# Kernel optimization log

Measured on AMD Instinct MI355X. Metric: run time of the kernel, lower is better.

The kernel has to match this reference:

```python
import jax, jax.numpy as jnp
import numpy as np

# World configuration (2D layout ['h','w'])
B = 16            # batch
NH, NW = 64, 64   # token grid (token_sizes)
DO = 768          # dim_in + dim_coords
KH, KW = 16, 16   # kernel_sizes (patch extent, overlapping)
SH, SW = 8, 8     # patch_sizes (strides)
H, WF = 512, 512  # field_sizes
E = H * WF        # world.num_elements


def _build_fold_index():
    # idx[h, w, dh, dw] = clamp(h*SH+dh, 0, H-1)*WF + clamp(w*SW+dw, 0, WF-1)
    # mirrors FieldDecoder._build_fold_index with grid strides (WF, 1)
    ph = np.clip(np.arange(NH)[:, None] * SH + np.arange(KH)[None, :], 0, H - 1)   # [NH,KH]
    pw = np.clip(np.arange(NW)[:, None] * SW + np.arange(KW)[None, :], 0, WF - 1)  # [NW,KW]
    idx = ph[:, None, :, None] * WF + pw[None, :, None, :]                          # [NH,NW,KH,KW]
    return jnp.asarray(idx.reshape(-1), dtype=jnp.int32)


def setup_inputs() -> dict:
    key = jax.random.key(0)
    k1, k2 = jax.random.split(key)
    tgt = jax.random.normal(k1, (B, NH * NW, DO), dtype=jnp.float32)
    weight = jax.random.normal(k2, (KH, KW, DO), dtype=jnp.float32) * 0.02  # EinMix weight (k=v=1 absorbed)
    idx = _build_fold_index()
    return {"tgt": tgt, "weight": weight, "idx": idx}


def reference(tgt, weight, idx):
    # EinMix: 'b (h w) do -> b (h w hh ww)'  (shared per-patch projection, k=v=1)
    proj = jnp.einsum('bnd,xyd->bnxy', tgt, weight)          # [B, NH*NW, KH, KW]
    proj = proj.reshape(B, -1)                                # flat order (h, w, hh, ww) == idx layout
    # scatter_reduce(reduce='mean', include_self=False): sum then divide by counts
    sums = jnp.zeros((B, E), proj.dtype).at[:, idx].add(proj)
    counts = jnp.zeros((E,), proj.dtype).at[idx].add(1.0)     # every element is covered (kernel >= stride)
    field = sums / jnp.maximum(counts, 1.0)
    # unflatten_fields: 'b (flat) -> b h w'
    return field.reshape(B, H, WF)
```

## Files before the change

kernel.cpp:

```cpp
#include <hip/hip_runtime.h>
#include <hip/hip_bf16.h>

#define DIM      768
#define NPATCH   4096
#define BATCH    16
#define MROWS    65536
#define NCOLS    256

typedef __attribute__((ext_vector_type(8))) short bf16x8;
typedef __attribute__((ext_vector_type(4))) float f32x4;
typedef unsigned short ushort_t;

static __device__ __forceinline__ unsigned short f2bf(float f) {
    union { float f; unsigned int u; } v; v.f = f;
    unsigned int u = v.u;
    return (unsigned short)((u + 0x7FFFu + ((u >> 16) & 1u)) >> 16);
}
static __device__ __forceinline__ float bf2f(unsigned int u16) {
    union { unsigned int i; float f; } x; x.i = u16 << 16; return x.f;
}

__global__ void wconv_kernel(const float* __restrict__ w, unsigned short* __restrict__ wb) {
    int i = blockIdx.x * blockDim.x + threadIdx.x;
    float4 v = ((const float4*)w)[i];
    unsigned int p0 = (unsigned)f2bf(v.x) | ((unsigned)f2bf(v.y) << 16);
    unsigned int p1 = (unsigned)f2bf(v.z) | ((unsigned)f2bf(v.w) << 16);
    ((uint2*)wb)[i] = make_uint2(p0, p1);
}

#define KHALF 384
#define LSTRA 392
#define CSTR  264

__global__ __launch_bounds__(256, 3) void gemm_kernel(const float* __restrict__ A,
                                                      const unsigned short* __restrict__ Bw,
                                                      unsigned short* __restrict__ Cb) {
    __shared__ unsigned short sA[64 * LSTRA];

    const int tid  = threadIdx.x;
    const int m0   = blockIdx.x * 64;
    const int wave = tid >> 6;
    const int lane = tid & 63;
    const int l15  = lane & 15;
    const int quad = lane >> 4;
    const int n0w  = wave * 64;

    f32x4 acc[4][4] = {};

    const int srow = tid >> 2;
    const int su   = tid & 3;

    const unsigned short* bBase[4];
    #pragma unroll
    for (int j = 0; j < 4; ++j)
        bBase[j] = Bw + (size_t)(n0w + j * 16 + l15) * DIM + quad * 8;
    const unsigned short* aBase = sA + l15 * LSTRA + quad * 8;

    for (int half = 0; half < 2; ++half) {
        const int kbase = half * KHALF;
        __syncthreads();
        {
            const float* aRow = A + (size_t)(m0 + srow) * DIM + kbase + su * 4;
            unsigned short* dRow = sA + srow * LSTRA + su * 4;
            #pragma unroll
            for (int p = 0; p < 24; ++p) {
                float4 v = *(const float4*)(aRow + p * 16);
                unsigned int p0 = (unsigned)f2bf(v.x) | ((unsigned)f2bf(v.y) << 16);
                unsigned int p1 = (unsigned)f2bf(v.z) | ((unsigned)f2bf(v.w) << 16);
                *(uint2*)(dRow + p * 16) = make_uint2(p0, p1);
            }
        }
        __syncthreads();

        #pragma unroll 4
        for (int kk = 0; kk < 12; ++kk) {
            bf16x8 bfr[4];
            #pragma unroll
            for (int j = 0; j < 4; ++j)
                bfr[j] = *(const bf16x8*)(bBase[j] + kbase + kk * 32);
            bf16x8 af[4];
            #pragma unroll
            for (int i = 0; i < 4; ++i)
                af[i] = *(const bf16x8*)(aBase + i * 16 * LSTRA + kk * 32);
            #pragma unroll
            for (int i = 0; i < 4; ++i)
                #pragma unroll
                for (int j = 0; j < 4; ++j)
                    acc[i][j] = __builtin_amdgcn_mfma_f32_16x16x32_bf16(af[i], bfr[j], acc[i][j], 0, 0, 0);
        }
    }

    __syncthreads();
    unsigned short* sC = sA;
    #pragma unroll
    for (int i = 0; i < 4; ++i)
        #pragma unroll
        for (int j = 0; j < 4; ++j)
            #pragma unroll
            for (int rr = 0; rr < 4; ++rr)
                sC[(i * 16 + quad * 4 + rr) * CSTR + n0w + j * 16 + l15] = f2bf(acc[i][j][rr]);
    __syncthreads();

    const int orow = tid >> 2;
    const int ou   = tid & 3;
    #pragma unroll
    for (int p = 0; p < 8; ++p) {
        uint4 v = *(const uint4*)(&sC[orow * CSTR + ou * 64 + p * 8]);
        *(uint4*)(Cb + (size_t)(m0 + orow) * NCOLS + ou * 64 + p * 8) = v;
    }
}

__global__ __launch_bounds__(256) void gather_kernel(const unsigned short* __restrict__ proj,
                                                     float* __restrict__ out) {
    __shared__ unsigned short sPrev[64 * 256];
    __shared__ unsigned short sCur[64 * 256];

    const int blk = blockIdx.x;
    const int b   = blk >> 6;
    const int h   = blk & 63;
    const int tid = threadIdx.x;
    const unsigned short* base = proj + (size_t)b * (NPATCH * NCOLS);

    const uint4* gCur = (const uint4*)(base + (size_t)h * 64 * 256);
    #pragma unroll
    for (int p = 0; p < 8; ++p)
        ((uint4*)sCur)[tid + p * 256] = gCur[tid + p * 256];
    if (h > 0) {
        const uint4* gPrev = (const uint4*)(base + (size_t)(h - 1) * 64 * 256);
        #pragma unroll
        for (int p = 0; p < 8; ++p)
            ((uint4*)sPrev)[tid + p * 256] = gPrev[tid + p * 256];
    }
    __syncthreads();

    const int r  = tid >> 5;
    const int cg = tid & 31;
    const int ph = h * 8 + r;

    auto tapW = [&](const unsigned short* row, int dh, int pw) -> float {
        const int w1 = pw >> 3, dw = pw & 7;
        float v = bf2f(row[w1 * 256 + dh * 16 + dw]);
        if (pw >= 8)
            v += bf2f(row[(w1 - 1) * 256 + dh * 16 + dw + 8]);
        if (pw == 511) {
            #pragma unroll
            for (int dwe = 8; dwe < 16; ++dwe)
                v += bf2f(row[63 * 256 + dh * 16 + dwe]);
        }
        return v;
    };

    const float inv_ch = (h == 0) ? 1.f : ((ph == 511) ? 0.1f : 0.5f);

    float res[16];
    #pragma unroll
    for (int j = 0; j < 16; ++j) {
        const int pw = cg * 16 + j;
        float v = tapW(sCur, r, pw);
        if (h > 0) v += tapW(sPrev, r + 8, pw);
        if (ph == 511) {
            #pragma unroll
            for (int dh = 8; dh < 16; ++dh) v += tapW(sCur, dh, pw);
        }
        const float inv_cw = (pw < 8) ? 1.f : ((pw == 511) ? 0.1f : 0.5f);
        res[j] = v * inv_ch * inv_cw;
    }

    float* orow = out + ((size_t)(b * 512 + ph)) * 512 + cg * 16;
    #pragma unroll
    for (int q = 0; q < 4; ++q)
        *(float4*)(orow + q * 4) = make_float4(res[4 * q], res[4 * q + 1], res[4 * q + 2], res[4 * q + 3]);
}

extern "C" void kernel_launch(void* const* d_in, const int* in_sizes, int n_in,
                              void* d_out, int out_size, void* d_ws, size_t ws_size,
                              hipStream_t stream) {
    const float* tgt    = (const float*)d_in[0];
    const float* weight = (const float*)d_in[1];
    float* out = (float*)d_out;

    unsigned short* proj = (unsigned short*)d_ws;
    unsigned short* wbf  = (unsigned short*)((char*)d_ws + (size_t)MROWS * NCOLS * 2);

    wconv_kernel<<<192, 256, 0, stream>>>(weight, wbf);
    gemm_kernel<<<MROWS / 64, 256, 0, stream>>>(tgt, wbf, proj);
    gather_kernel<<<BATCH * 64, 256, 0, stream>>>(proj, out);
}
```

Measured before the change: 371.9 us.

## Shrink GEMM tile to 32 rows with K-chunking; load only needed prev-row half in gather

The GEMM now uses a 32-row M tile and streams the K dimension in six 128-wide chunks through a small LDS buffer, which cuts registers and LDS so more blocks fit per CU (launch bound raised to 6). The trade is twice as many blocks and more reloads of the weight fragments, plus a barrier per chunk with no overlap of loads and compute. The gather kernel now loads only the lower-half kernel rows (dh 8..15) of the previous patch row, halving that global read and its LDS footprint.

```diff
diff --git a/kernel.cpp b/kernel.cpp
--- a/kernel.cpp
+++ b/kernel.cpp
@@ -9,7 +9,6 @@
 
 typedef __attribute__((ext_vector_type(8))) short bf16x8;
 typedef __attribute__((ext_vector_type(4))) float f32x4;
-typedef unsigned short ushort_t;
 
 static __device__ __forceinline__ unsigned short f2bf(float f) {
     union { float f; unsigned int u; } v; v.f = f;
@@ -28,92 +27,85 @@
     ((uint2*)wb)[i] = make_uint2(p0, p1);
 }
 
-#define KHALF 384
-#define LSTRA 392
-#define CSTR  264
+#define CHUNK 128
+#define LSTC  136
 
-__global__ __launch_bounds__(256, 3) void gemm_kernel(const float* __restrict__ A,
+__global__ __launch_bounds__(256, 6) void gemm_kernel(const float* __restrict__ A,
                                                       const unsigned short* __restrict__ Bw,
                                                       unsigned short* __restrict__ Cb) {
-    __shared__ unsigned short sA[64 * LSTRA];
+    __shared__ unsigned short smem[32 * 256];
 
     const int tid  = threadIdx.x;
-    const int m0   = blockIdx.x * 64;
-    const int wave = tid >> 6;
+    const int m0   = blockIdx.x * 32;
+    const int wv   = tid >> 6;
     const int lane = tid & 63;
     const int l15  = lane & 15;
     const int quad = lane >> 4;
-    const int n0w  = wave * 64;
 
-    f32x4 acc[4][4] = {};
-
-    const int srow = tid >> 2;
-    const int su   = tid & 3;
+    f32x4 acc[2][4] = {};
 
     const unsigned short* bBase[4];
     #pragma unroll
     for (int j = 0; j < 4; ++j)
-        bBase[j] = Bw + (size_t)(n0w + j * 16 + l15) * DIM + quad * 8;
-    const unsigned short* aBase = sA + l15 * LSTRA + quad * 8;
+        bBase[j] = Bw + (size_t)(wv * 64 + j * 16 + l15) * DIM + quad * 8;
+    const unsigned short* aFrag0 = smem + l15 * LSTC + quad * 8;
+    const unsigned short* aFrag1 = aFrag0 + 16 * LSTC;
 
-    for (int half = 0; half < 2; ++half) {
-        const int kbase = half * KHALF;
+    const int srow = tid >> 3;
+    const int su   = tid & 7;
+    const float* aSrc = A + (size_t)(m0 + srow) * DIM + su * 4;
+    unsigned short* aDst = smem + srow * LSTC + su * 4;
+
+    for (int c = 0; c < 6; ++c) {
+        const int kb = c * CHUNK;
         __syncthreads();
-        {
-            const float* aRow = A + (size_t)(m0 + srow) * DIM + kbase + su * 4;
-            unsigned short* dRow = sA + srow * LSTRA + su * 4;
-            #pragma unroll
-            for (int p = 0; p < 24; ++p) {
-                float4 v = *(const float4*)(aRow + p * 16);
-                unsigned int p0 = (unsigned)f2bf(v.x) | ((unsigned)f2bf(v.y) << 16);
-                unsigned int p1 = (unsigned)f2bf(v.z) | ((unsigned)f2bf(v.w) << 16);
-                *(uint2*)(dRow + p * 16) = make_uint2(p0, p1);
-            }
+        #pragma unroll
+        for (int p = 0; p < 4; ++p) {
+            float4 v = *(const float4*)(aSrc + kb + p * 32);
+            unsigned int p0 = (unsigned)f2bf(v.x) | ((unsigned)f2bf(v.y) << 16);
+            unsigned int p1 = (unsigned)f2bf(v.z) | ((unsigned)f2bf(v.w) << 16);
+            *(uint2*)(aDst + p * 32) = make_uint2(p0, p1);
         }
         __syncthreads();
-
-        #pragma unroll 4
-        for (int kk = 0; kk < 12; ++kk) {
-            bf16x8 bfr[4];
+        #pragma unroll
+        for (int kk = 0; kk < 4; ++kk) {
+            bf16x8 bf[4];
             #pragma unroll
             for (int j = 0; j < 4; ++j)
-                bfr[j] = *(const bf16x8*)(bBase[j] + kbase + kk * 32);
-            bf16x8 af[4];
+                bf[j] = *(const bf16x8*)(bBase[j] + kb + kk * 32);
+            bf16x8 a0 = *(const bf16x8*)(aFrag0 + kk * 32);
+            bf16x8 a1 = *(const bf16x8*)(aFrag1 + kk * 32);
             #pragma unroll
-            for (int i = 0; i < 4; ++i)
-                af[i] = *(const bf16x8*)(aBase + i * 16 * LSTRA + kk * 32);
-            #pragma unroll
-            for (int i = 0; i < 4; ++i)
-                #pragma unroll
-                for (int j = 0; j < 4; ++j)
-                    acc[i][j] = __builtin_amdgcn_mfma_f32_16x16x32_bf16(af[i], bfr[j], acc[i][j], 0, 0, 0);
+            for (int j = 0; j < 4; ++j) {
+                acc[0][j] = __builtin_amdgcn_mfma_f32_16x16x32_bf16(a0, bf[j], acc[0][j], 0, 0, 0);
+                acc[1][j] = __builtin_amdgcn_mfma_f32_16x16x32_bf16(a1, bf[j], acc[1][j], 0, 0, 0);
+            }
         }
     }
 
     __syncthreads();
-    unsigned short* sC = sA;
     #pragma unroll
-    for (int i = 0; i < 4; ++i)
+    for (int i = 0; i < 2; ++i)
         #pragma unroll
         for (int j = 0; j < 4; ++j)
             #pragma unroll
             for (int rr = 0; rr < 4; ++rr)
-                sC[(i * 16 + quad * 4 + rr) * CSTR + n0w + j * 16 + l15] = f2bf(acc[i][j][rr]);
+                smem[(i * 16 + quad * 4 + rr) * 256 + wv * 64 + j * 16 + l15] = f2bf(acc[i][j][rr]);
     __syncthreads();
 
-    const int orow = tid >> 2;
-    const int ou   = tid & 3;
+    const int orow = tid >> 3;
+    const int ou   = tid & 7;
     #pragma unroll
-    for (int p = 0; p < 8; ++p) {
-        uint4 v = *(const uint4*)(&sC[orow * CSTR + ou * 64 + p * 8]);
-        *(uint4*)(Cb + (size_t)(m0 + orow) * NCOLS + ou * 64 + p * 8) = v;
+    for (int q = 0; q < 4; ++q) {
+        uint4 v = *(const uint4*)(smem + orow * 256 + ou * 32 + q * 8);
+        *(uint4*)(Cb + (size_t)(m0 + orow) * NCOLS + ou * 32 + q * 8) = v;
     }
 }
 
 __global__ __launch_bounds__(256) void gather_kernel(const unsigned short* __restrict__ proj,
                                                      float* __restrict__ out) {
-    __shared__ unsigned short sPrev[64 * 256];
     __shared__ unsigned short sCur[64 * 256];
+    __shared__ unsigned short sPrevHi[64 * 128];
 
     const int blk = blockIdx.x;
     const int b   = blk >> 6;
@@ -128,39 +120,48 @@
     if (h > 0) {
         const uint4* gPrev = (const uint4*)(base + (size_t)(h - 1) * 64 * 256);
         #pragma unroll
-        for (int p = 0; p < 8; ++p)
-            ((uint4*)sPrev)[tid + p * 256] = gPrev[tid + p * 256];
+        for (int p = 0; p < 4; ++p) {
+            int i = tid + p * 256;
+            ((uint4*)sPrevHi)[i] = gPrev[(i >> 4) * 32 + 16 + (i & 15)];
+        }
     }
     __syncthreads();
 
     const int r  = tid >> 5;
     const int cg = tid & 31;
     const int ph = h * 8 + r;
-
-    auto tapW = [&](const unsigned short* row, int dh, int pw) -> float {
-        const int w1 = pw >> 3, dw = pw & 7;
-        float v = bf2f(row[w1 * 256 + dh * 16 + dw]);
-        if (pw >= 8)
-            v += bf2f(row[(w1 - 1) * 256 + dh * 16 + dw + 8]);
-        if (pw == 511) {
-            #pragma unroll
-            for (int dwe = 8; dwe < 16; ++dwe)
-                v += bf2f(row[63 * 256 + dh * 16 + dwe]);
-        }
-        return v;
-    };
-
     const float inv_ch = (h == 0) ? 1.f : ((ph == 511) ? 0.1f : 0.5f);
 
     float res[16];
     #pragma unroll
     for (int j = 0; j < 16; ++j) {
         const int pw = cg * 16 + j;
-        float v = tapW(sCur, r, pw);
-        if (h > 0) v += tapW(sPrev, r + 8, pw);
+        const int w1 = pw >> 3, dw = pw & 7;
+        float v = bf2f(sCur[w1 * 256 + r * 16 + dw]);
+        if (pw >= 8) v += bf2f(sCur[(w1 - 1) * 256 + r * 16 + dw + 8]);
+        if (h > 0) {
+            v += bf2f(sPrevHi[w1 * 128 + r * 16 + dw]);
+            if (pw >= 8) v += bf2f(sPrevHi[(w1 - 1) * 128 + r * 16 + dw + 8]);
+        }
+        if (pw == 511) {
+            #pragma unroll
+            for (int dwe = 8; dwe < 16; ++dwe) {
+                v += bf2f(sCur[63 * 256 + r * 16 + dwe]);
+                if (h > 0) v += bf2f(sPrevHi[63 * 128 + r * 16 + dwe]);
+            }
+        }
         if (ph == 511) {
-            #pragma unroll
-            for (int dh = 8; dh < 16; ++dh) v += tapW(sCur, dh, pw);
+            #pragma unroll 1
+            for (int dh = 8; dh < 16; ++dh) {
+                float e = bf2f(sCur[w1 * 256 + dh * 16 + dw]);
+                if (pw >= 8) e += bf2f(sCur[(w1 - 1) * 256 + dh * 16 + dw + 8]);
+                if (pw == 511) {
+                    #pragma unroll
+                    for (int dwe = 8; dwe < 16; ++dwe)
+                        e += bf2f(sCur[63 * 256 + dh * 16 + dwe]);
+                }
+                v += e;
+            }
         }
         const float inv_cw = (pw < 8) ? 1.f : ((pw == 511) ? 0.1f : 0.5f);
         res[j] = v * inv_ch * inv_cw;
@@ -183,6 +184,6 @@
     unsigned short* wbf  = (unsigned short*)((char*)d_ws + (size_t)MROWS * NCOLS * 2);
 
     wconv_kernel<<<192, 256, 0, stream>>>(weight, wbf);
-    gemm_kernel<<<MROWS / 64, 256, 0, stream>>>(tgt, wbf, proj);
+    gemm_kernel<<<MROWS / 32, 256, 0, stream>>>(tgt, wbf, proj);
     gather_kernel<<<BATCH * 64, 256, 0, stream>>>(proj, out);
 }
```

New measurement: 421.7 us. 13.4% more time.
